# Kernel optimization log

Measured on AMD Instinct MI355X. Metric: run time of the kernel, lower is better.

The kernel has to match this reference:

```python
import jax, jax.numpy as jnp
import numpy as np

N = 50000
E = 1600000
IN_DIM = 128
BN_EPS = 1e-5
NEG_SLOPE = 0.2


def _gat_layer(x, src, dst, W, a_s, a_d, b):
    """PyG GATConv (concat heads, eval mode). x:[N,F], src/dst:[E'], W:[F,H*C]."""
    H, C = a_s.shape
    n = x.shape[0]
    h = (x @ W).reshape(n, H, C)                        # [N,H,C]
    al_s = jnp.einsum('nhc,hc->nh', h, a_s)             # per-node src logits
    al_d = jnp.einsum('nhc,hc->nh', h, a_d)             # per-node dst logits
    e = jax.nn.leaky_relu(al_s[src] + al_d[dst], NEG_SLOPE)  # [E',H]
    m = jax.ops.segment_max(e, dst, num_segments=n)
    m = jnp.where(jnp.isfinite(m), m, 0.0)
    ex = jnp.exp(e - m[dst])
    denom = jax.ops.segment_sum(ex, dst, num_segments=n)
    alpha = ex / (denom[dst] + 1e-16)                   # segment softmax over incoming edges
    msg = alpha[:, :, None] * h[src]                    # [E',H,C]
    out = jax.ops.segment_sum(msg, dst, num_segments=n) # [N,H,C]
    return out.reshape(n, H * C) + b


def _bn(x, g, b, m, v):
    return (x - m) * jax.lax.rsqrt(v + BN_EPS) * g + b


def setup_inputs() -> dict:
    key = jax.random.key(0)
    ks = jax.random.split(key, 16)
    d = {}
    d['x'] = jax.random.normal(ks[0], (N, IN_DIM), jnp.float32)
    d['edge_index'] = jax.random.randint(ks[1], (2, E), 0, N, dtype=jnp.int32)
    def glorot(k, shape):
        fan = shape[0] + shape[-1]
        return jax.random.normal(k, shape, jnp.float32) * np.sqrt(2.0 / fan)
    d['W1'] = glorot(ks[2], (IN_DIM, 64)); d['a_src1'] = glorot(ks[3], (4, 16)); d['a_dst1'] = glorot(ks[4], (4, 16)); d['b1'] = jnp.zeros((64,), jnp.float32)
    d['bn1_g'] = jnp.ones((64,), jnp.float32); d['bn1_b'] = jnp.zeros((64,), jnp.float32); d['bn1_m'] = jnp.zeros((64,), jnp.float32); d['bn1_v'] = jnp.ones((64,), jnp.float32)
    d['W2'] = glorot(ks[5], (64, 64)); d['a_src2'] = glorot(ks[6], (4, 16)); d['a_dst2'] = glorot(ks[7], (4, 16)); d['b2'] = jnp.zeros((64,), jnp.float32)
    d['bn2_g'] = jnp.ones((64,), jnp.float32); d['bn2_b'] = jnp.zeros((64,), jnp.float32); d['bn2_m'] = jnp.zeros((64,), jnp.float32); d['bn2_v'] = jnp.ones((64,), jnp.float32)
    d['W3'] = glorot(ks[8], (64, 16)); d['a_src3'] = glorot(ks[9], (1, 16)); d['a_dst3'] = glorot(ks[10], (1, 16)); d['b3'] = jnp.zeros((16,), jnp.float32)
    d['bn3_g'] = jnp.ones((16,), jnp.float32); d['bn3_b'] = jnp.zeros((16,), jnp.float32); d['bn3_m'] = jnp.zeros((16,), jnp.float32); d['bn3_v'] = jnp.ones((16,), jnp.float32)
    d['fc1_w'] = glorot(ks[11], (16, 8)); d['fc1_b'] = jnp.zeros((8,), jnp.float32)
    d['fc2_w'] = glorot(ks[12], (8, 1)); d['fc2_b'] = jnp.zeros((1,), jnp.float32)
    return d


def reference(x, edge_index, W1, a_src1, a_dst1, b1, bn1_g, bn1_b, bn1_m, bn1_v,
              W2, a_src2, a_dst2, b2, bn2_g, bn2_b, bn2_m, bn2_v,
              W3, a_src3, a_dst3, b3, bn3_g, bn3_b, bn3_m, bn3_v,
              fc1_w, fc1_b, fc2_w, fc2_b):
    n = x.shape[0]
    loops = jnp.arange(n, dtype=edge_index.dtype)       # PyG GATConv adds self-loops
    src = jnp.concatenate([edge_index[0], loops])
    dst = jnp.concatenate([edge_index[1], loops])

    h = _gat_layer(x, src, dst, W1, a_src1, a_dst1, b1)
    h = jax.nn.relu(_bn(h, bn1_g, bn1_b, bn1_m, bn1_v))
    h = _gat_layer(h, src, dst, W2, a_src2, a_dst2, b2)
    h = jax.nn.relu(_bn(h, bn2_g, bn2_b, bn2_m, bn2_v))
    h = _gat_layer(h, src, dst, W3, a_src3, a_dst3, b3)
    h = jax.nn.relu(_bn(h, bn3_g, bn3_b, bn3_m, bn3_v))
    h = jax.nn.relu(h @ fc1_w + fc1_b)
    return h @ fc2_w + fc2_b                            # [N,1]
```

## Files before the change

kernel.cpp:

```cpp
#include <hip/hip_runtime.h>
#include <hip/hip_fp16.h>

#define IN_DIM 128
#define SLW 64
#define SLSH 6
#define CAPS 3072
#define EPA 2048
#define MAXSL 1024

__device__ __forceinline__ float lrelu(float x) { return x > 0.f ? x : 0.2f * x; }

template<int F>
__global__ __launch_bounds__(256, 4) void gemm64_al_kernel(const float* __restrict__ in,
                                                           const float* __restrict__ W,
                                                           const float* __restrict__ a_s,
                                                           const float* __restrict__ a_d,
                                                           __half* __restrict__ h16,
                                                           float* __restrict__ als,
                                                           float* __restrict__ ald, int n) {
    constexpr int KT = 64;
    constexpr int XS = KT + 4;
    __shared__ float wl[KT * 64];
    __shared__ float xl[64 * XS];
    const int t = threadIdx.x;
    const int node0 = blockIdx.x * 64;
    const int tn = t >> 4;
    const int tc = t & 15;
    float4 acc[4] = {{0,0,0,0},{0,0,0,0},{0,0,0,0},{0,0,0,0}};

#pragma unroll 1
    for (int kt = 0; kt < F; kt += KT) {
        for (int idx = t * 4; idx < KT * 64; idx += 1024)
            *(float4*)&wl[idx] = *(const float4*)(W + kt * 64 + idx);
        for (int idx = t * 4; idx < 64 * KT; idx += 1024) {
            int node = idx >> 6, k = idx & 63;
            float4 v = make_float4(0.f, 0.f, 0.f, 0.f);
            if (node0 + node < n) v = *(const float4*)(in + (size_t)(node0 + node) * F + kt + k);
            *(float4*)&xl[node * XS + k] = v;
        }
        __syncthreads();

        for (int k0 = 0; k0 < KT; k0 += 4) {
            float4 xa[4];
#pragma unroll
            for (int i = 0; i < 4; ++i) xa[i] = *(const float4*)&xl[(tn * 4 + i) * XS + k0];
#pragma unroll
            for (int kk = 0; kk < 4; ++kk) {
                float4 wv = *(const float4*)&wl[(k0 + kk) * 64 + tc * 4];
#pragma unroll
                for (int i = 0; i < 4; ++i) {
                    float xv = (kk == 0) ? xa[i].x : (kk == 1) ? xa[i].y : (kk == 2) ? xa[i].z : xa[i].w;
                    acc[i].x = fmaf(xv, wv.x, acc[i].x);
                    acc[i].y = fmaf(xv, wv.y, acc[i].y);
                    acc[i].z = fmaf(xv, wv.z, acc[i].z);
                    acc[i].w = fmaf(xv, wv.w, acc[i].w);
                }
            }
        }
        __syncthreads();
    }

    const float4 asv = *(const float4*)(a_s + tc * 4);
    const float4 adv = *(const float4*)(a_d + tc * 4);
#pragma unroll
    for (int i = 0; i < 4; ++i) {
        int node = node0 + tn * 4 + i;
        float ps = acc[i].x * asv.x + acc[i].y * asv.y + acc[i].z * asv.z + acc[i].w * asv.w;
        float pd = acc[i].x * adv.x + acc[i].y * adv.y + acc[i].z * adv.z + acc[i].w * adv.w;
        ps += __shfl_xor(ps, 1, 64); ps += __shfl_xor(ps, 2, 64);
        pd += __shfl_xor(pd, 1, 64); pd += __shfl_xor(pd, 2, 64);
        if (node < n) {
            __half2 p0 = __floats2half2_rn(acc[i].x, acc[i].y);
            __half2 p1 = __floats2half2_rn(acc[i].z, acc[i].w);
            int2 pk;
            pk.x = *(int*)&p0;
            pk.y = *(int*)&p1;
            *(int2*)(h16 + ((size_t)node << 6) + (tc << 2)) = pk;
            if ((t & 3) == 0) {
                int hd = tc >> 2;
                als[node * 4 + hd] = ps;
                ald[node * 4 + hd] = pd;
            }
        }
    }
}

template<int F, int HC, int H>
__global__ __launch_bounds__(256) void gemm_al_kernel(const float* __restrict__ in,
                                                      const float* __restrict__ W,
                                                      const float* __restrict__ a_s,
                                                      const float* __restrict__ a_d,
                                                      float* __restrict__ h,
                                                      float* __restrict__ als,
                                                      float* __restrict__ ald, int n) {
    constexpr int NPB = 256 / HC;
    __shared__ float wl[F * HC];
    __shared__ float xl[NPB * F];
    const int t = threadIdx.x;
    for (int i = t; i < F * HC; i += 256) wl[i] = W[i];
    const int node0 = blockIdx.x * NPB;
    for (int i = t; i < NPB * F; i += 256) {
        int node = node0 + i / F;
        xl[i] = (node < n) ? in[node * F + (i % F)] : 0.f;
    }
    __syncthreads();
    const int nl = t / HC, col = t % HC;
    const int node = node0 + nl;
    if (node >= n) return;
    float acc = 0.f;
#pragma unroll
    for (int k = 0; k < F; ++k) acc += xl[nl * F + k] * wl[k * HC + col];
    h[node * HC + col] = acc;
    float ps = acc * a_s[col];
    float pd = acc * a_d[col];
#pragma unroll
    for (int msk = 1; msk < 16; msk <<= 1) {
        ps += __shfl_xor(ps, msk, 64);
        pd += __shfl_xor(pd, msk, 64);
    }
    if ((col & 15) == 0) {
        int head = col >> 4;
        als[node * H + head] = ps;
        ald[node * H + head] = pd;
    }
}

__global__ __launch_bounds__(256) void partition_kernel(const int* __restrict__ ei,
                                                        int* __restrict__ scur,
                                                        int* __restrict__ pairs,
                                                        int ne, int n, int nsl) {
    constexpr int EPT = EPA / 256;
    __shared__ int lcnt[MAXSL], lbase[MAXSL], lcur[MAXSL];
    const int t = threadIdx.x;
    for (int i = t; i < MAXSL; i += 256) lcnt[i] = 0;
    __syncthreads();
    const int base = blockIdx.x * EPA;
    const int end = min(ne + n, base + EPA);
    int pk[EPT];
#pragma unroll
    for (int k = 0; k < EPT; ++k) {
        int e = base + t + k * 256;
        if (e < end) {
            int s, d;
            if (e < ne) { s = ei[e]; d = ei[ne + e]; } else { s = d = e - ne; }
            pk[k] = (d << 16) | s;
            atomicAdd(&lcnt[d >> SLSH], 1);
        }
    }
    __syncthreads();
    for (int s = t; s < nsl; s += 256) {
        lbase[s] = lcnt[s] ? atomicAdd(scur + s, lcnt[s]) : 0;
        lcur[s] = 0;
    }
    __syncthreads();
#pragma unroll
    for (int k = 0; k < EPT; ++k) {
        int e = base + t + k * 256;
        if (e < end) {
            int sl = ((unsigned)pk[k]) >> (16 + SLSH);
            int pos = lbase[sl] + atomicAdd(&lcur[sl], 1);
            if (pos < CAPS) pairs[(size_t)sl * CAPS + pos] = pk[k];
        }
    }
}

__global__ __launch_bounds__(1024) void sscan_kernel(const int* __restrict__ scur,
                                                     int* __restrict__ sbase, int nsl) {
    __shared__ int sh[1024];
    int t = threadIdx.x;
    int v = (t < nsl) ? scur[t] : 0;
    int orig = v;
    sh[t] = v;
    __syncthreads();
    for (int o = 1; o < 1024; o <<= 1) {
        int other = (t >= o) ? sh[t - o] : 0;
        __syncthreads();
        v += other;
        sh[t] = v;
        __syncthreads();
    }
    if (t < nsl) sbase[t] = v - orig;
}

__global__ __launch_bounds__(256) void buildcsr_kernel(const int* __restrict__ pairs,
                                                       const int* __restrict__ scur,
                                                       const int* __restrict__ sbase,
                                                       int* __restrict__ csr,
                                                       int* __restrict__ off,
                                                       int n, int et, int nsl) {
    __shared__ int hist[SLW], hoff[SLW], hcur[SLW];
    __shared__ int lcsr[CAPS];
    __shared__ int hs[SLW];
    const int sl = blockIdx.x;
    const int lo = sl << SLSH;
    const int cnt = min(scur[sl], CAPS);
    const int gbase = sbase[sl];
    const int t = threadIdx.x;
    const int* pp = pairs + (size_t)sl * CAPS;
    if (t < SLW) { hist[t] = 0; hcur[t] = 0; }
    __syncthreads();
    for (int i = t; i < cnt; i += 256) atomicAdd(&hist[(((unsigned)pp[i]) >> 16) - lo], 1);
    __syncthreads();
    if (t < SLW) hs[t] = hist[t];
    __syncthreads();
    for (int o = 1; o < SLW; o <<= 1) {
        int val = (t < SLW && t >= o) ? hs[t - o] : 0;
        __syncthreads();
        if (t < SLW) hs[t] += val;
        __syncthreads();
    }
    if (t < SLW) hoff[t] = hs[t] - hist[t];
    __syncthreads();
    if (t < SLW && lo + t < n) off[lo + t] = gbase + hoff[t];
    if (sl == nsl - 1 && t == 0) off[n] = et;
    for (int i = t; i < cnt; i += 256) {
        int p = pp[i];
        int dl = (((unsigned)p) >> 16) - lo;
        int r = atomicAdd(&hcur[dl], 1);
        lcsr[hoff[dl] + r] = p & 0xFFFF;
    }
    __syncthreads();
    for (int i = t; i < cnt; i += 256) csr[gbase + i] = lcsr[i];
}

__global__ __launch_bounds__(256) void agg64_kernel(const int* __restrict__ off,
                                                    const int* __restrict__ csr,
                                                    const float* __restrict__ als,
                                                    const float* __restrict__ ald,
                                                    const __half* __restrict__ h16,
                                                    const float* __restrict__ bias,
                                                    const float* __restrict__ g,
                                                    const float* __restrict__ bb,
                                                    const float* __restrict__ mm,
                                                    const float* __restrict__ vv,
                                                    float* __restrict__ feat, int n) {
    const int wpair = (blockIdx.x * blockDim.x + threadIdx.x) >> 6;
    const int lane = threadIdx.x & 63;
    const int dstA = wpair << 1;
    if (dstA >= n) return;
    const int dstB = min(dstA + 1, n - 1);

    const int ha = lane & 3;
    const int el = lane >> 2;
    const int c4 = lane & 15;
    const int hd = c4 >> 2;
    const int eg = lane >> 4;

    const int startA = off[dstA];
    const int degA = off[dstA + 1] - startA;
    const int startB = off[dstB];
    const int degB = off[dstB + 1] - startB;
    const float aldaA = ald[(dstA << 2) + ha];
    const float aldaB = ald[(dstB << 2) + ha];

    float4 accA = {0.f, 0.f, 0.f, 0.f}, accB = {0.f, 0.f, 0.f, 0.f};
    float lsumA = 0.f, lsumB = 0.f;
    const int maxdeg = max(degA, degB);

    for (int i = 0; i < maxdeg; i += 16) {
        const int slot = i + el;
        int sA = csr[startA + min(slot, degA - 1)];
        int sB = csr[startB + min(slot, degB - 1)];
        float wA = __expf(lrelu(als[(sA << 2) + ha] + aldaA));
        float wB = __expf(lrelu(als[(sB << 2) + ha] + aldaB));
        wA = (slot < degA) ? wA : 0.f;
        wB = (slot < degB) ? wB : 0.f;
        lsumA += wA;
        lsumB += wB;
#pragma unroll
        for (int j0 = 0; j0 < 16; j0 += 4) {
            int srcl = ((j0 + eg) << 2) + hd;
            float wjA = __shfl(wA, srcl, 64);
            int sjA = __shfl(sA, srcl, 64);
            float wjB = __shfl(wB, srcl, 64);
            int sjB = __shfl(sB, srcl, 64);
            const int2 hpA = *(const int2*)(h16 + ((size_t)sjA << 6) + (c4 << 2));
            const int2 hpB = *(const int2*)(h16 + ((size_t)sjB << 6) + (c4 << 2));
            const float2 a0 = __half22float2(*(const __half2*)&hpA.x);
            const float2 a1 = __half22float2(*(const __half2*)&hpA.y);
            const float2 b0 = __half22float2(*(const __half2*)&hpB.x);
            const float2 b1 = __half22float2(*(const __half2*)&hpB.y);
            accA.x = fmaf(wjA, a0.x, accA.x);
            accA.y = fmaf(wjA, a0.y, accA.y);
            accA.z = fmaf(wjA, a1.x, accA.z);
            accA.w = fmaf(wjA, a1.y, accA.w);
            accB.x = fmaf(wjB, b0.x, accB.x);
            accB.y = fmaf(wjB, b0.y, accB.y);
            accB.z = fmaf(wjB, b1.x, accB.z);
            accB.w = fmaf(wjB, b1.y, accB.w);
        }
    }

#pragma unroll
    for (int msk = 4; msk < 64; msk <<= 1) {
        lsumA += __shfl_xor(lsumA, msk, 64);
        lsumB += __shfl_xor(lsumB, msk, 64);
    }
    const float denomA = __shfl(lsumA, hd, 64);
    const float denomB = __shfl(lsumB, hd, 64);
#pragma unroll
    for (int msk = 16; msk < 64; msk <<= 1) {
        accA.x += __shfl_xor(accA.x, msk, 64);
        accA.y += __shfl_xor(accA.y, msk, 64);
        accA.z += __shfl_xor(accA.z, msk, 64);
        accA.w += __shfl_xor(accA.w, msk, 64);
        accB.x += __shfl_xor(accB.x, msk, 64);
        accB.y += __shfl_xor(accB.y, msk, 64);
        accB.z += __shfl_xor(accB.z, msk, 64);
        accB.w += __shfl_xor(accB.w, msk, 64);
    }
    if (lane < 32) {
        const int cb = c4 << 2;
        const float4 bi = *(const float4*)(bias + cb);
        const float4 gg = *(const float4*)(g + cb);
        const float4 bbv = *(const float4*)(bb + cb);
        const float4 mmv = *(const float4*)(mm + cb);
        const float4 vvv = *(const float4*)(vv + cb);
        const bool isA = lane < 16;
        const float4 acc = isA ? accA : accB;
        const float inv = 1.f / ((isA ? denomA : denomB) + 1e-16f);
        const int dst = isA ? dstA : dstB;
        float4 o;
        o.x = fmaxf((acc.x * inv + bi.x - mmv.x) * rsqrtf(vvv.x + 1e-5f) * gg.x + bbv.x, 0.f);
        o.y = fmaxf((acc.y * inv + bi.y - mmv.y) * rsqrtf(vvv.y + 1e-5f) * gg.y + bbv.y, 0.f);
        o.z = fmaxf((acc.z * inv + bi.z - mmv.z) * rsqrtf(vvv.z + 1e-5f) * gg.z + bbv.z, 0.f);
        o.w = fmaxf((acc.w * inv + bi.w - mmv.w) * rsqrtf(vvv.w + 1e-5f) * gg.w + bbv.w, 0.f);
        *(float4*)(feat + ((size_t)dst << 6) + cb) = o;
    }
}

__global__ __launch_bounds__(256) void agg16_mlp_kernel(const int* __restrict__ off,
                                                        const int* __restrict__ csr,
                                                        const float* __restrict__ als,
                                                        const float* __restrict__ ald,
                                                        const float* __restrict__ h,
                                                        const float* __restrict__ bias,
                                                        const float* __restrict__ g,
                                                        const float* __restrict__ bb,
                                                        const float* __restrict__ mm,
                                                        const float* __restrict__ vv,
                                                        const float* __restrict__ fc1w,
                                                        const float* __restrict__ fc1b,
                                                        const float* __restrict__ fc2w,
                                                        const float* __restrict__ fc2b,
                                                        float* __restrict__ out, int n) {
    const int wpair = (blockIdx.x * blockDim.x + threadIdx.x) >> 6;
    const int lane = threadIdx.x & 63;
    const int dstA = wpair << 1;
    if (dstA >= n) return;
    const int dstB = min(dstA + 1, n - 1);

    const int startA = off[dstA];
    const int degA = off[dstA + 1] - startA;
    const int startB = off[dstB];
    const int degB = off[dstB + 1] - startB;
    const float aldvA = ald[dstA];
    const float aldvB = ald[dstB];

    const int eg = lane >> 4, c = lane & 15;
    float accA = 0.f, accB = 0.f, lsumA = 0.f, lsumB = 0.f;
    const int maxdeg = max(degA, degB);

    for (int i = 0; i < maxdeg; i += 16) {
        const int slot = i + (lane & 15);
        int sA = csr[startA + min(slot, degA - 1)];
        int sB = csr[startB + min(slot, degB - 1)];
        float wA = __expf(lrelu(als[sA] + aldvA));
        float wB = __expf(lrelu(als[sB] + aldvB));
        wA = (slot < degA) ? wA : 0.f;
        wB = (slot < degB) ? wB : 0.f;
        if (eg == 0) { lsumA += wA; lsumB += wB; }
#pragma unroll
        for (int jj = 0; jj < 16; jj += 4) {
            int j = jj + eg;
            float wjA = __shfl(wA, j, 64);
            int sjA = __shfl(sA, j, 64);
            float wjB = __shfl(wB, j, 64);
            int sjB = __shfl(sB, j, 64);
            accA = fmaf(wjA, h[(sjA << 4) + c], accA);
            accB = fmaf(wjB, h[(sjB << 4) + c], accB);
        }
    }
#pragma unroll
    for (int msk = 1; msk < 16; msk <<= 1) {
        lsumA += __shfl_xor(lsumA, msk, 64);
        lsumB += __shfl_xor(lsumB, msk, 64);
    }
    lsumA = __shfl(lsumA, c & 15, 64);
    lsumB = __shfl(lsumB, c & 15, 64);
#pragma unroll
    for (int msk = 16; msk < 64; msk <<= 1) {
        accA += __shfl_xor(accA, msk, 64);
        accB += __shfl_xor(accB, msk, 64);
    }
    if (lane < 32) {
        const bool isA = lane < 16;
        const float acc = isA ? accA : accB;
        const float lsum = isA ? lsumA : lsumB;
        float val = acc / (lsum + 1e-16f) + bias[c];
        val = (val - mm[c]) * rsqrtf(vv[c] + 1e-5f) * g[c] + bb[c];
        val = fmaxf(val, 0.f);
        float p[8];
#pragma unroll
        for (int j = 0; j < 8; ++j) p[j] = val * fc1w[c * 8 + j];
#pragma unroll
        for (int msk = 1; msk < 16; msk <<= 1) {
#pragma unroll
            for (int j = 0; j < 8; ++j) p[j] += __shfl_xor(p[j], msk, 64);
        }
        if (c == 0) {
            const int dst = isA ? dstA : dstB;
            float o = fc2b[0];
#pragma unroll
            for (int j = 0; j < 8; ++j) {
                float hv = fmaxf(p[j] + fc1b[j], 0.f);
                o = fmaf(hv, fc2w[j], o);
            }
            out[dst] = o;
        }
    }
}

extern "C" void kernel_launch(void* const* d_in, const int* in_sizes, int n_in,
                              void* d_out, int out_size, void* d_ws, size_t ws_size,
                              hipStream_t stream) {
    const float* x    = (const float*)d_in[0];
    const int*   ei   = (const int*)d_in[1];
    const float* W1   = (const float*)d_in[2];
    const float* As1  = (const float*)d_in[3];
    const float* Ad1  = (const float*)d_in[4];
    const float* b1   = (const float*)d_in[5];
    const float* bn1g = (const float*)d_in[6];
    const float* bn1b = (const float*)d_in[7];
    const float* bn1m = (const float*)d_in[8];
    const float* bn1v = (const float*)d_in[9];
    const float* W2   = (const float*)d_in[10];
    const float* As2  = (const float*)d_in[11];
    const float* Ad2  = (const float*)d_in[12];
    const float* b2   = (const float*)d_in[13];
    const float* bn2g = (const float*)d_in[14];
    const float* bn2b = (const float*)d_in[15];
    const float* bn2m = (const float*)d_in[16];
    const float* bn2v = (const float*)d_in[17];
    const float* W3   = (const float*)d_in[18];
    const float* As3  = (const float*)d_in[19];
    const float* Ad3  = (const float*)d_in[20];
    const float* b3   = (const float*)d_in[21];
    const float* bn3g = (const float*)d_in[22];
    const float* bn3b = (const float*)d_in[23];
    const float* bn3m = (const float*)d_in[24];
    const float* bn3v = (const float*)d_in[25];
    const float* fc1w = (const float*)d_in[26];
    const float* fc1b = (const float*)d_in[27];
    const float* fc2w = (const float*)d_in[28];
    const float* fc2b = (const float*)d_in[29];

    const int n  = in_sizes[0] / IN_DIM;
    const int ne = in_sizes[1] / 2;
    const int et = ne + n;
    const int nsl = (n + SLW - 1) >> SLSH;

    float* hbase = (float*)d_ws;
    __half* h16  = (__half*)hbase;
    float* h3    = hbase + (size_t)n * 32;
    float* feat  = hbase + (size_t)n * 64;
    float* als   = feat + (size_t)n * 64;
    float* ald   = als + (size_t)n * 4;
    int* pairs   = (int*)(ald + (size_t)n * 4);
    int* scur    = pairs + (size_t)nsl * CAPS;
    int* sbase   = scur + nsl;
    int* off     = sbase + nsl;
    int* csr     = off + (n + 1);

    auto cdiv = [](long a, long b) { return (int)((a + b - 1) / b); };

    hipMemsetAsync(scur, 0, (size_t)nsl * sizeof(int), stream);
    partition_kernel<<<cdiv(et, EPA), 256, 0, stream>>>(ei, scur, pairs, ne, n, nsl);
    sscan_kernel<<<1, 1024, 0, stream>>>(scur, sbase, nsl);
    buildcsr_kernel<<<nsl, 256, 0, stream>>>(pairs, scur, sbase, csr, off, n, et, nsl);

    gemm64_al_kernel<128><<<cdiv(n, 64), 256, 0, stream>>>(x, W1, As1, Ad1, h16, als, ald, n);
    agg64_kernel<<<cdiv(n, 8), 256, 0, stream>>>(off, csr, als, ald, h16,
        b1, bn1g, bn1b, bn1m, bn1v, feat, n);

    gemm64_al_kernel<64><<<cdiv(n, 64), 256, 0, stream>>>(feat, W2, As2, Ad2, h16, als, ald, n);
    agg64_kernel<<<cdiv(n, 8), 256, 0, stream>>>(off, csr, als, ald, h16,
        b2, bn2g, bn2b, bn2m, bn2v, feat, n);

    gemm_al_kernel<64, 16, 1><<<cdiv(n, 16), 256, 0, stream>>>(feat, W3, As3, Ad3, h3, als, ald, n);
    agg16_mlp_kernel<<<cdiv(n, 8), 256, 0, stream>>>(off, csr, als, ald, h3,
        b3, bn3g, bn3b, bn3m, bn3v, fc1w, fc1b, fc2w, fc2b, (float*)d_out, n);
}
```

Baseline: 316.9 us.

## Fuse edge partition with first GEMM and fold segment scan into CSR build

Merges the edge-partition kernel and the layer-1 GEMM into one launch, where block indices choose which body runs, so the two independent stages can overlap on the GPU. Removes the single-block scan kernel: each CSR-build block now computes its own global base by reducing the preceding segment counts. This saves two launches and a serial step, at the cost of redundant reduction work in every buildcsr block and a larger shared-memory footprint for the partition blocks.

```diff
diff --git a/kernel.cpp b/kernel.cpp
--- a/kernel.cpp
+++ b/kernel.cpp
@@ -7,23 +7,24 @@
 #define CAPS 3072
 #define EPA 2048
 #define MAXSL 1024
+#define SMEMB 33792
 
 __device__ __forceinline__ float lrelu(float x) { return x > 0.f ? x : 0.2f * x; }
 
 template<int F>
-__global__ __launch_bounds__(256, 4) void gemm64_al_kernel(const float* __restrict__ in,
-                                                           const float* __restrict__ W,
-                                                           const float* __restrict__ a_s,
-                                                           const float* __restrict__ a_d,
-                                                           __half* __restrict__ h16,
-                                                           float* __restrict__ als,
-                                                           float* __restrict__ ald, int n) {
+__device__ __forceinline__ void gemm64_body(char* smem_, int node0,
+                                            const float* __restrict__ in,
+                                            const float* __restrict__ W,
+                                            const float* __restrict__ a_s,
+                                            const float* __restrict__ a_d,
+                                            __half* __restrict__ h16,
+                                            float* __restrict__ als,
+                                            float* __restrict__ ald, int n) {
     constexpr int KT = 64;
     constexpr int XS = KT + 4;
-    __shared__ float wl[KT * 64];
-    __shared__ float xl[64 * XS];
+    float* wl = (float*)smem_;
+    float* xl = wl + KT * 64;
     const int t = threadIdx.x;
-    const int node0 = blockIdx.x * 64;
     const int tn = t >> 4;
     const int tc = t & 15;
     float4 acc[4] = {{0,0,0,0},{0,0,0,0},{0,0,0,0},{0,0,0,0}};
@@ -85,6 +86,78 @@
     }
 }
 
+__device__ __forceinline__ void partition_body(char* smem_, int bid,
+                                               const int* __restrict__ ei,
+                                               int* __restrict__ scur,
+                                               int* __restrict__ pairs,
+                                               int ne, int n, int nsl) {
+    constexpr int EPT = EPA / 256;
+    int* lcnt  = (int*)smem_;
+    int* lbase = lcnt + MAXSL;
+    int* lcur  = lbase + MAXSL;
+    const int t = threadIdx.x;
+    for (int i = t; i < MAXSL; i += 256) lcnt[i] = 0;
+    __syncthreads();
+    const int base = bid * EPA;
+    const int end = min(ne + n, base + EPA);
+    int pk[EPT];
+#pragma unroll
+    for (int k = 0; k < EPT; ++k) {
+        int e = base + t + k * 256;
+        if (e < end) {
+            int s, d;
+            if (e < ne) { s = ei[e]; d = ei[ne + e]; } else { s = d = e - ne; }
+            pk[k] = (d << 16) | s;
+            atomicAdd(&lcnt[d >> SLSH], 1);
+        }
+    }
+    __syncthreads();
+    for (int s = t; s < nsl; s += 256) {
+        lbase[s] = lcnt[s] ? atomicAdd(scur + s, lcnt[s]) : 0;
+        lcur[s] = 0;
+    }
+    __syncthreads();
+#pragma unroll
+    for (int k = 0; k < EPT; ++k) {
+        int e = base + t + k * 256;
+        if (e < end) {
+            int sl = ((unsigned)pk[k]) >> (16 + SLSH);
+            int pos = lbase[sl] + atomicAdd(&lcur[sl], 1);
+            if (pos < CAPS) pairs[(size_t)sl * CAPS + pos] = pk[k];
+        }
+    }
+}
+
+__global__ __launch_bounds__(256, 4) void part_gemm1_kernel(const int* __restrict__ ei,
+                                                            int* __restrict__ scur,
+                                                            int* __restrict__ pairs,
+                                                            int ne, int nsl, int npart,
+                                                            const float* __restrict__ in,
+                                                            const float* __restrict__ W,
+                                                            const float* __restrict__ a_s,
+                                                            const float* __restrict__ a_d,
+                                                            __half* __restrict__ h16,
+                                                            float* __restrict__ als,
+                                                            float* __restrict__ ald, int n) {
+    __shared__ __align__(16) char smem_[SMEMB];
+    if ((int)blockIdx.x < npart)
+        partition_body(smem_, blockIdx.x, ei, scur, pairs, ne, n, nsl);
+    else
+        gemm64_body<IN_DIM>(smem_, (blockIdx.x - npart) * 64, in, W, a_s, a_d, h16, als, ald, n);
+}
+
+template<int F>
+__global__ __launch_bounds__(256, 4) void gemm64_al_kernel(const float* __restrict__ in,
+                                                           const float* __restrict__ W,
+                                                           const float* __restrict__ a_s,
+                                                           const float* __restrict__ a_d,
+                                                           __half* __restrict__ h16,
+                                                           float* __restrict__ als,
+                                                           float* __restrict__ ald, int n) {
+    __shared__ __align__(16) char smem_[SMEMB];
+    gemm64_body<F>(smem_, blockIdx.x * 64, in, W, a_s, a_d, h16, als, ald, n);
+}
+
 template<int F, int HC, int H>
 __global__ __launch_bounds__(256) void gemm_al_kernel(const float* __restrict__ in,
                                                       const float* __restrict__ W,
@@ -125,77 +198,28 @@
     }
 }
 
-__global__ __launch_bounds__(256) void partition_kernel(const int* __restrict__ ei,
-                                                        int* __restrict__ scur,
-                                                        int* __restrict__ pairs,
-                                                        int ne, int n, int nsl) {
-    constexpr int EPT = EPA / 256;
-    __shared__ int lcnt[MAXSL], lbase[MAXSL], lcur[MAXSL];
-    const int t = threadIdx.x;
-    for (int i = t; i < MAXSL; i += 256) lcnt[i] = 0;
-    __syncthreads();
-    const int base = blockIdx.x * EPA;
-    const int end = min(ne + n, base + EPA);
-    int pk[EPT];
-#pragma unroll
-    for (int k = 0; k < EPT; ++k) {
-        int e = base + t + k * 256;
-        if (e < end) {
-            int s, d;
-            if (e < ne) { s = ei[e]; d = ei[ne + e]; } else { s = d = e - ne; }
-            pk[k] = (d << 16) | s;
-            atomicAdd(&lcnt[d >> SLSH], 1);
-        }
-    }
-    __syncthreads();
-    for (int s = t; s < nsl; s += 256) {
-        lbase[s] = lcnt[s] ? atomicAdd(scur + s, lcnt[s]) : 0;
-        lcur[s] = 0;
-    }
-    __syncthreads();
-#pragma unroll
-    for (int k = 0; k < EPT; ++k) {
-        int e = base + t + k * 256;
-        if (e < end) {
-            int sl = ((unsigned)pk[k]) >> (16 + SLSH);
-            int pos = lbase[sl] + atomicAdd(&lcur[sl], 1);
-            if (pos < CAPS) pairs[(size_t)sl * CAPS + pos] = pk[k];
-        }
-    }
-}
-
-__global__ __launch_bounds__(1024) void sscan_kernel(const int* __restrict__ scur,
-                                                     int* __restrict__ sbase, int nsl) {
-    __shared__ int sh[1024];
-    int t = threadIdx.x;
-    int v = (t < nsl) ? scur[t] : 0;
-    int orig = v;
-    sh[t] = v;
-    __syncthreads();
-    for (int o = 1; o < 1024; o <<= 1) {
-        int other = (t >= o) ? sh[t - o] : 0;
-        __syncthreads();
-        v += other;
-        sh[t] = v;
-        __syncthreads();
-    }
-    if (t < nsl) sbase[t] = v - orig;
-}
-
 __global__ __launch_bounds__(256) void buildcsr_kernel(const int* __restrict__ pairs,
                                                        const int* __restrict__ scur,
-                                                       const int* __restrict__ sbase,
                                                        int* __restrict__ csr,
                                                        int* __restrict__ off,
                                                        int n, int et, int nsl) {
     __shared__ int hist[SLW], hoff[SLW], hcur[SLW];
+    __shared__ int hs[SLW];
+    __shared__ int red[256];
     __shared__ int lcsr[CAPS];
-    __shared__ int hs[SLW];
     const int sl = blockIdx.x;
     const int lo = sl << SLSH;
+    const int t = threadIdx.x;
+    int part = 0;
+    for (int i = t; i < sl; i += 256) part += scur[i];
+    red[t] = part;
+    __syncthreads();
+    for (int o = 128; o > 0; o >>= 1) {
+        if (t < o) red[t] += red[t + o];
+        __syncthreads();
+    }
+    const int gbase = red[0];
     const int cnt = min(scur[sl], CAPS);
-    const int gbase = sbase[sl];
-    const int t = threadIdx.x;
     const int* pp = pairs + (size_t)sl * CAPS;
     if (t < SLW) { hist[t] = 0; hcur[t] = 0; }
     __syncthreads();
@@ -468,18 +492,18 @@
     float* ald   = als + (size_t)n * 4;
     int* pairs   = (int*)(ald + (size_t)n * 4);
     int* scur    = pairs + (size_t)nsl * CAPS;
-    int* sbase   = scur + nsl;
-    int* off     = sbase + nsl;
+    int* off     = scur + nsl;
     int* csr     = off + (n + 1);
 
     auto cdiv = [](long a, long b) { return (int)((a + b - 1) / b); };
+    const int npart = cdiv(et, EPA);
+    const int ngemm = cdiv(n, 64);
 
     hipMemsetAsync(scur, 0, (size_t)nsl * sizeof(int), stream);
-    partition_kernel<<<cdiv(et, EPA), 256, 0, stream>>>(ei, scur, pairs, ne, n, nsl);
-    sscan_kernel<<<1, 1024, 0, stream>>>(scur, sbase, nsl);
-    buildcsr_kernel<<<nsl, 256, 0, stream>>>(pairs, scur, sbase, csr, off, n, et, nsl);
-
-    gemm64_al_kernel<128><<<cdiv(n, 64), 256, 0, stream>>>(x, W1, As1, Ad1, h16, als, ald, n);
+    part_gemm1_kernel<<<npart + ngemm, 256, 0, stream>>>(ei, scur, pairs, ne, nsl, npart,
+                                                         x, W1, As1, Ad1, h16, als, ald, n);
+    buildcsr_kernel<<<nsl, 256, 0, stream>>>(pairs, scur, csr, off, n, et, nsl);
+
     agg64_kernel<<<cdiv(n, 8), 256, 0, stream>>>(off, csr, als, ald, h16,
         b1, bn1g, bn1b, bn1m, bn1v, feat, n);
 
```

New measurement: 310.1 us. 1.02x faster.

## Replace bucketed CSR build with global count, scan, atomic scatter

Applied to the files above, without the earlier changes.

Swaps the two-level slice-partition CSR construction (LDS histograms, per-slice pair buckets, per-slice local sort) for a plain per-node count with global atomics, a single-block serial-per-thread scan, and an atomic-cursor scatter. It removes the intermediate pairs buffer and its CAPS truncation. In exchange it uses many contended global atomics, writes the CSR in scattered order, and runs a scan in one block where each thread loops over about 49 nodes. Edge order within a node's list becomes nondeterministic, which changes floating-point summation order.

```diff
diff --git a/kernel.cpp b/kernel.cpp
--- a/kernel.cpp
+++ b/kernel.cpp
@@ -2,11 +2,6 @@
 #include <hip/hip_fp16.h>
 
 #define IN_DIM 128
-#define SLW 64
-#define SLSH 6
-#define CAPS 3072
-#define EPA 2048
-#define MAXSL 1024
 
 __device__ __forceinline__ float lrelu(float x) { return x > 0.f ? x : 0.2f * x; }
 
@@ -125,102 +120,59 @@
     }
 }
 
-__global__ __launch_bounds__(256) void partition_kernel(const int* __restrict__ ei,
-                                                        int* __restrict__ scur,
-                                                        int* __restrict__ pairs,
-                                                        int ne, int n, int nsl) {
-    constexpr int EPT = EPA / 256;
-    __shared__ int lcnt[MAXSL], lbase[MAXSL], lcur[MAXSL];
+__global__ __launch_bounds__(256) void count_kernel(const int* __restrict__ ei,
+                                                    int* __restrict__ cnt,
+                                                    int ne, int et) {
+    for (int e = blockIdx.x * 2048 + threadIdx.x, k = 0; k < 8; ++k, e += 256) {
+        if (e < et) {
+            int d = (e < ne) ? ei[ne + e] : (e - ne);
+            atomicAdd(&cnt[d], 1);
+        }
+    }
+}
+
+__global__ __launch_bounds__(1024) void scan_kernel(const int* __restrict__ cnt,
+                                                    int* __restrict__ off,
+                                                    int* __restrict__ cur,
+                                                    int n, int et) {
+    __shared__ int bs[1024];
     const int t = threadIdx.x;
-    for (int i = t; i < MAXSL; i += 256) lcnt[i] = 0;
+    const int per = (n + 1023) >> 10;
+    const int begin = t * per;
+    const int end = min(begin + per, n);
+    int s = 0;
+    for (int i = begin; i < end; ++i) s += cnt[i];
+    bs[t] = s;
     __syncthreads();
-    const int base = blockIdx.x * EPA;
-    const int end = min(ne + n, base + EPA);
-    int pk[EPT];
-#pragma unroll
-    for (int k = 0; k < EPT; ++k) {
-        int e = base + t + k * 256;
-        if (e < end) {
+    int v = s;
+    for (int o = 1; o < 1024; o <<= 1) {
+        int other = (t >= o) ? bs[t - o] : 0;
+        __syncthreads();
+        v += other;
+        bs[t] = v;
+        __syncthreads();
+    }
+    int base = v - s;
+    for (int i = begin; i < end; ++i) {
+        off[i] = base;
+        cur[i] = base;
+        base += cnt[i];
+    }
+    if (t == 0) off[n] = et;
+}
+
+__global__ __launch_bounds__(256) void scatter_kernel(const int* __restrict__ ei,
+                                                      int* __restrict__ cur,
+                                                      int* __restrict__ csr,
+                                                      int ne, int et) {
+    for (int e = blockIdx.x * 2048 + threadIdx.x, k = 0; k < 8; ++k, e += 256) {
+        if (e < et) {
             int s, d;
             if (e < ne) { s = ei[e]; d = ei[ne + e]; } else { s = d = e - ne; }
-            pk[k] = (d << 16) | s;
-            atomicAdd(&lcnt[d >> SLSH], 1);
-        }
-    }
-    __syncthreads();
-    for (int s = t; s < nsl; s += 256) {
-        lbase[s] = lcnt[s] ? atomicAdd(scur + s, lcnt[s]) : 0;
-        lcur[s] = 0;
-    }
-    __syncthreads();
-#pragma unroll
-    for (int k = 0; k < EPT; ++k) {
-        int e = base + t + k * 256;
-        if (e < end) {
-            int sl = ((unsigned)pk[k]) >> (16 + SLSH);
-            int pos = lbase[sl] + atomicAdd(&lcur[sl], 1);
-            if (pos < CAPS) pairs[(size_t)sl * CAPS + pos] = pk[k];
-        }
-    }
-}
-
-__global__ __launch_bounds__(1024) void sscan_kernel(const int* __restrict__ scur,
-                                                     int* __restrict__ sbase, int nsl) {
-    __shared__ int sh[1024];
-    int t = threadIdx.x;
-    int v = (t < nsl) ? scur[t] : 0;
-    int orig = v;
-    sh[t] = v;
-    __syncthreads();
-    for (int o = 1; o < 1024; o <<= 1) {
-        int other = (t >= o) ? sh[t - o] : 0;
-        __syncthreads();
-        v += other;
-        sh[t] = v;
-        __syncthreads();
-    }
-    if (t < nsl) sbase[t] = v - orig;
-}
-
-__global__ __launch_bounds__(256) void buildcsr_kernel(const int* __restrict__ pairs,
-                                                       const int* __restrict__ scur,
-                                                       const int* __restrict__ sbase,
-                                                       int* __restrict__ csr,
-                                                       int* __restrict__ off,
-                                                       int n, int et, int nsl) {
-    __shared__ int hist[SLW], hoff[SLW], hcur[SLW];
-    __shared__ int lcsr[CAPS];
-    __shared__ int hs[SLW];
-    const int sl = blockIdx.x;
-    const int lo = sl << SLSH;
-    const int cnt = min(scur[sl], CAPS);
-    const int gbase = sbase[sl];
-    const int t = threadIdx.x;
-    const int* pp = pairs + (size_t)sl * CAPS;
-    if (t < SLW) { hist[t] = 0; hcur[t] = 0; }
-    __syncthreads();
-    for (int i = t; i < cnt; i += 256) atomicAdd(&hist[(((unsigned)pp[i]) >> 16) - lo], 1);
-    __syncthreads();
-    if (t < SLW) hs[t] = hist[t];
-    __syncthreads();
-    for (int o = 1; o < SLW; o <<= 1) {
-        int val = (t < SLW && t >= o) ? hs[t - o] : 0;
-        __syncthreads();
-        if (t < SLW) hs[t] += val;
-        __syncthreads();
-    }
-    if (t < SLW) hoff[t] = hs[t] - hist[t];
-    __syncthreads();
-    if (t < SLW && lo + t < n) off[lo + t] = gbase + hoff[t];
-    if (sl == nsl - 1 && t == 0) off[n] = et;
-    for (int i = t; i < cnt; i += 256) {
-        int p = pp[i];
-        int dl = (((unsigned)p) >> 16) - lo;
-        int r = atomicAdd(&hcur[dl], 1);
-        lcsr[hoff[dl] + r] = p & 0xFFFF;
-    }
-    __syncthreads();
-    for (int i = t; i < cnt; i += 256) csr[gbase + i] = lcsr[i];
+            int pos = atomicAdd(&cur[d], 1);
+            csr[pos] = s;
+        }
+    }
 }
 
 __global__ __launch_bounds__(256) void agg64_kernel(const int* __restrict__ off,
@@ -458,7 +410,6 @@
     const int n  = in_sizes[0] / IN_DIM;
     const int ne = in_sizes[1] / 2;
     const int et = ne + n;
-    const int nsl = (n + SLW - 1) >> SLSH;
 
     float* hbase = (float*)d_ws;
     __half* h16  = (__half*)hbase;
@@ -466,18 +417,17 @@
     float* feat  = hbase + (size_t)n * 64;
     float* als   = feat + (size_t)n * 64;
     float* ald   = als + (size_t)n * 4;
-    int* pairs   = (int*)(ald + (size_t)n * 4);
-    int* scur    = pairs + (size_t)nsl * CAPS;
-    int* sbase   = scur + nsl;
-    int* off     = sbase + nsl;
+    int* cnt     = (int*)(ald + (size_t)n * 4);
+    int* cur     = cnt + n;
+    int* off     = cur + n;
     int* csr     = off + (n + 1);
 
     auto cdiv = [](long a, long b) { return (int)((a + b - 1) / b); };
 
-    hipMemsetAsync(scur, 0, (size_t)nsl * sizeof(int), stream);
-    partition_kernel<<<cdiv(et, EPA), 256, 0, stream>>>(ei, scur, pairs, ne, n, nsl);
-    sscan_kernel<<<1, 1024, 0, stream>>>(scur, sbase, nsl);
-    buildcsr_kernel<<<nsl, 256, 0, stream>>>(pairs, scur, sbase, csr, off, n, et, nsl);
+    hipMemsetAsync(cnt, 0, (size_t)n * sizeof(int), stream);
+    count_kernel<<<cdiv(et, 2048), 256, 0, stream>>>(ei, cnt, ne, et);
+    scan_kernel<<<1, 1024, 0, stream>>>(cnt, off, cur, n, et);
+    scatter_kernel<<<cdiv(et, 2048), 256, 0, stream>>>(ei, cur, csr, ne, et);
 
     gemm64_al_kernel<128><<<cdiv(n, 64), 256, 0, stream>>>(x, W1, As1, Ad1, h16, als, ald, n);
     agg64_kernel<<<cdiv(n, 8), 256, 0, stream>>>(off, csr, als, ald, h16,
```

Result: slower. 585.9 us (+84.9%).
